# Optimization experiments

Measured on AMD Instinct MI355X. Metric: run time of the kernel, lower is better.

Reference implementation:

```python
import jax, jax.numpy as jnp
import numpy as np

B, T, C = 1, 2048, 1024
H, D = 16, 64  # n_head, head_size (n_query_groups == n_head -> plain MHA)


def build_rope_cache(seq_len, n_elem, base=10000):
    theta = 1.0 / (base ** (jnp.arange(0, n_elem, 2, dtype=jnp.float32) / n_elem))
    idx_theta = jnp.outer(jnp.arange(seq_len, dtype=jnp.float32), theta)
    idx_theta = jnp.concatenate([idx_theta, idx_theta], axis=-1)  # torch .repeat(1, 2)
    return jnp.cos(idx_theta), jnp.sin(idx_theta)


def apply_rope(x, cos, sin):
    d = x.shape[-1]
    x1, x2 = x[..., : d // 2], x[..., d // 2 :]
    rotated = jnp.concatenate([-x2, x1], axis=-1)
    return x * cos + rotated * sin


def fastmax_attention(q, k, v):
    """Fastmax: first-order Taylor approx of softmax attention, causal, O(n*d^2).
    score(i,j) = 1 + q_i . k_j (temperature=1, zero RPE, no dropout);
    out_i = sum_{j<=i} score*v_j / sum_{j<=i} score, via causal cumulative sums."""
    n = q.shape[2]
    kcum = jnp.cumsum(k, axis=2)                                       # (B,H,T,D)
    kvcum = jnp.cumsum(jnp.einsum('bhnd,bhne->bhnde', k, v), axis=2)   # (B,H,T,D,D)
    den = jnp.arange(1, n + 1, dtype=q.dtype) + jnp.einsum('bhnd,bhnd->bhn', q, kcum)
    num = jnp.cumsum(v, axis=2) + jnp.einsum('bhnd,bhnde->bhne', q, kvcum)
    return num / den[..., None]


def setup_inputs() -> dict:
    key = jax.random.key(0)
    k1, k2, k3 = jax.random.split(key, 3)
    scale = 0.02
    x = jax.random.normal(k1, (B, T, C), dtype=jnp.float32)
    w_attn = jax.random.normal(k2, (3 * H * D, C), dtype=jnp.float32) * scale
    w_proj = jax.random.normal(k3, (C, H * D), dtype=jnp.float32) * scale
    cos, sin = build_rope_cache(T, D)
    return {"x": x, "w_attn": w_attn, "w_proj": w_proj, "cos": cos, "sin": sin}


def reference(x, w_attn, w_proj, cos, sin):
    Bx, Tx, Cx = x.shape
    qkv = x @ w_attn.T                                  # (B,T,3HD)
    qkv = qkv.reshape(Bx, Tx, H, 3, D).transpose(0, 2, 3, 1, 4)  # (B,H,3,T,D)
    q, k, v = qkv[:, :, 0], qkv[:, :, 1], qkv[:, :, 2]
    q = apply_rope(q, cos, sin)
    k = apply_rope(k, cos, sin)
    y = fastmax_attention(q, k, v)                      # (B,H,T,D)
    y = y.transpose(0, 2, 1, 3).reshape(Bx, Tx, H * D)
    return y @ w_proj.T
```

## Files before the change

kernel.cpp:

```cpp
#include <hip/hip_runtime.h>

#define T_LEN 2048
#define C_DIM 1024
#define H_NUM 16
#define D_DIM 64
#define QKV_N (3 * H_NUM * D_DIM)
#define L_CHK 64
#define NC (T_LEN / L_CHK)

typedef _Float16 h8 __attribute__((ext_vector_type(8)));
typedef _Float16 h4 __attribute__((ext_vector_type(4)));
typedef float f32x4 __attribute__((ext_vector_type(4)));

__global__ __launch_bounds__(256) void split3_f16(
    const float* __restrict__ x, _Float16* __restrict__ xh,
    _Float16* __restrict__ xl, const float* __restrict__ wa,
    _Float16* __restrict__ wah, _Float16* __restrict__ wal,
    const float* __restrict__ wp, _Float16* __restrict__ wph) {
  int i = (blockIdx.x * 256 + threadIdx.x) * 8;
  const float* src;
  _Float16 *dh, *dl = nullptr;
  int base;
  if (i < 2097152) {
    src = x; dh = xh; dl = xl; base = i;
  } else if (i < 2097152 + 3145728) {
    src = wa; dh = wah; dl = wal; base = i - 2097152;
  } else {
    src = wp; dh = wph; base = i - 5242880;
  }
  float4 a = *(const float4*)(src + base);
  float4 b = *(const float4*)(src + base + 4);
  float v[8] = {a.x, a.y, a.z, a.w, b.x, b.y, b.z, b.w};
  h8 hv, lv;
#pragma unroll
  for (int j = 0; j < 8; ++j) {
    float s = v[j] * 64.f;
    _Float16 h = (_Float16)s;
    hv[j] = h;
    lv[j] = (_Float16)(s - (float)h);
  }
  *(h8*)(dh + base) = hv;
  if (dl) *(h8*)(dl + base) = lv;
}

__device__ __forceinline__ void split8(float4 a, float4 b, h8& hi, h8& lo) {
  float v[8] = {a.x, a.y, a.z, a.w, b.x, b.y, b.z, b.w};
#pragma unroll
  for (int m = 0; m < 8; ++m) {
    _Float16 hh = (_Float16)v[m];
    hi[m] = hh;
    lo[m] = (_Float16)(v[m] - (float)hh);
  }
}

template <int BN, bool ROPE, bool SPLIT3>
__global__ __launch_bounds__(256) void gemm_nt_f16(
    const _Float16* __restrict__ Ah, const _Float16* __restrict__ Al,
    const _Float16* __restrict__ Bh, const _Float16* __restrict__ Bl,
    float* __restrict__ C, const float* __restrict__ cosb,
    const float* __restrict__ sinb, _Float16* __restrict__ qh_,
    _Float16* __restrict__ ql_, _Float16* __restrict__ kh_,
    _Float16* __restrict__ kl_, _Float16* __restrict__ kTh_,
    _Float16* __restrict__ kTl_, _Float16* __restrict__ vTh_,
    int M, int N, int K, float outscale) {
  constexpr int NJ = BN / 32;
  constexpr int NARR = SPLIT3 ? 2 : 1;
  constexpr int GEMM_BYTES = (64 * 64 * 2 + BN * 64 * 2) * NARR;
  constexpr int ROPE_BYTES = ROPE ? (2 * 64 * 36 * 4 + 2 * 64 * 64 * 4) : 0;
  constexpr int SMEM_BYTES = GEMM_BYTES > ROPE_BYTES ? GEMM_BYTES : ROPE_BYTES;
  __shared__ __align__(16) char smem[SMEM_BYTES];
  _Float16* sAh = (_Float16*)smem;
  _Float16* sAl = sAh + 64 * 64;
  _Float16* sBh = sAh + 64 * 64 * NARR;
  _Float16* sBl = sBh + BN * 64;
  const int tid = threadIdx.x;
  const int wave = tid >> 6;
  const int lane = tid & 63;
  const int bm = blockIdx.y * 64;
  const int bn = blockIdx.x * BN;
  const int wm = wave >> 1;
  const int wn = wave & 1;
  const int srow = lane >> 3;
  const int sblk = ((lane & 7) ^ srow) * 8;
  const int quad = lane >> 4;
  const int lrow = lane & 15;

  f32x4 acc[2][NJ];
#pragma unroll
  for (int i = 0; i < 2; ++i)
#pragma unroll
    for (int j = 0; j < NJ; ++j) acc[i][j] = (f32x4){0.f, 0.f, 0.f, 0.f};

  for (int k0 = 0; k0 < K; k0 += 64) {
#pragma unroll
    for (int it = 0; it < 2; ++it) {
      const int ch = wave + it * 4;
      const int row = ch * 8 + srow;
      const _Float16* ga = Ah + (size_t)(bm + row) * K + k0 + sblk;
      __builtin_amdgcn_global_load_lds(
          (const __attribute__((address_space(1))) void*)ga,
          (__attribute__((address_space(3))) void*)(sAh + ch * 512), 16, 0, 0);
      if constexpr (SPLIT3) {
        const _Float16* gb = Al + (size_t)(bm + row) * K + k0 + sblk;
        __builtin_amdgcn_global_load_lds(
            (const __attribute__((address_space(1))) void*)gb,
            (__attribute__((address_space(3))) void*)(sAl + ch * 512), 16, 0,
            0);
      }
    }
#pragma unroll
    for (int it = 0; it < BN / 32; ++it) {
      const int ch = wave + it * 4;
      const int row = ch * 8 + srow;
      const _Float16* ga = Bh + (size_t)(bn + row) * K + k0 + sblk;
      __builtin_amdgcn_global_load_lds(
          (const __attribute__((address_space(1))) void*)ga,
          (__attribute__((address_space(3))) void*)(sBh + ch * 512), 16, 0, 0);
      if constexpr (SPLIT3) {
        const _Float16* gb = Bl + (size_t)(bn + row) * K + k0 + sblk;
        __builtin_amdgcn_global_load_lds(
            (const __attribute__((address_space(1))) void*)gb,
            (__attribute__((address_space(3))) void*)(sBl + ch * 512), 16, 0,
            0);
      }
    }
    __syncthreads();
#pragma unroll
    for (int kk = 0; kk < 2; ++kk) {
      h8 ah[2], al[2], bh[NJ], bl[NJ];
#pragma unroll
      for (int i = 0; i < 2; ++i) {
        const int row = wm * 32 + i * 16 + lrow;
        const int ra = row * 64 + (((kk * 4 + quad) ^ (row & 7)) * 8);
        ah[i] = *(const h8*)&sAh[ra];
        if constexpr (SPLIT3) al[i] = *(const h8*)&sAl[ra];
      }
#pragma unroll
      for (int j = 0; j < NJ; ++j) {
        const int row = wn * (BN / 2) + j * 16 + lrow;
        const int rb = row * 64 + (((kk * 4 + quad) ^ (row & 7)) * 8);
        bh[j] = *(const h8*)&sBh[rb];
        if constexpr (SPLIT3) bl[j] = *(const h8*)&sBl[rb];
      }
#pragma unroll
      for (int i = 0; i < 2; ++i)
#pragma unroll
        for (int j = 0; j < NJ; ++j) {
          acc[i][j] = __builtin_amdgcn_mfma_f32_16x16x32_f16(
              ah[i], bh[j], acc[i][j], 0, 0, 0);
          if constexpr (SPLIT3) {
            acc[i][j] = __builtin_amdgcn_mfma_f32_16x16x32_f16(
                ah[i], bl[j], acc[i][j], 0, 0, 0);
            acc[i][j] = __builtin_amdgcn_mfma_f32_16x16x32_f16(
                al[i], bh[j], acc[i][j], 0, 0, 0);
          }
        }
    }
    __syncthreads();
  }
  if constexpr (!ROPE) {
#pragma unroll
    for (int i = 0; i < 2; ++i) {
      const int rbase = bm + wm * 32 + i * 16 + quad * 4;
#pragma unroll
      for (int j = 0; j < NJ; ++j) {
        const int col = bn + wn * (BN / 2) + j * 16 + lrow;
#pragma unroll
        for (int r = 0; r < 4; ++r)
          C[(size_t)(rbase + r) * N + col] = acc[i][j][r] * outscale;
      }
    }
  } else {
    float* cs = (float*)smem;
    float* sn = cs + 2304;
    float* bounce = sn + 2304;
    {
      const int el = tid * 8;
      const int t = el >> 5, d0 = el & 31;
      const float* gc = &cosb[(size_t)(bm + t) * D_DIM + d0];
      const float* gs = &sinb[(size_t)(bm + t) * D_DIM + d0];
      *(float4*)&cs[t * 36 + d0] = *(const float4*)gc;
      *(float4*)&cs[t * 36 + d0 + 4] = *(const float4*)(gc + 4);
      *(float4*)&sn[t * 36 + d0] = *(const float4*)gs;
      *(float4*)&sn[t * 36 + d0 + 4] = *(const float4*)(gs + 4);
    }
    __syncthreads();
    const int colbase = bn + wn * 64;
    const int type = (colbase >> 6) % 3;
    const int head = colbase / 192;
    const size_t hb = (size_t)head * T_LEN * D_DIM;
    float fv[2][4][4];
#pragma unroll
    for (int i = 0; i < 2; ++i)
#pragma unroll
      for (int r = 0; r < 4; ++r) {
        const int tloc = wm * 32 + i * 16 + quad * 4 + r;
#pragma unroll
        for (int j = 0; j < 4; ++j) {
          const int d32 = (j & 1) * 16 + lrow;
          float val = acc[i][j][r] * outscale;
          if (type < 2) {
            float rotv =
                ((j < 2) ? -acc[i][j + 2][r] : acc[i][j - 2][r]) * outscale;
            val = val * cs[tloc * 36 + d32] + rotv * sn[tloc * 36 + d32];
          }
          fv[i][r][j] = val;
        }
      }
    if (type < 2) {
      _Float16* dh = (type == 0 ? qh_ : kh_) + hb;
      _Float16* dl = (type == 0 ? ql_ : kl_) + hb;
#pragma unroll
      for (int i = 0; i < 2; ++i)
#pragma unroll
        for (int r = 0; r < 4; ++r) {
          const size_t trow =
              (size_t)(bm + wm * 32 + i * 16 + quad * 4 + r) * D_DIM;
#pragma unroll
          for (int j = 0; j < 4; ++j) {
            const int d = j * 16 + lrow;
            float f = fv[i][r][j];
            _Float16 hh = (_Float16)f;
            dh[trow + d] = hh;
            dl[trow + d] = (_Float16)(f - (float)hh);
          }
        }
    }
    const bool doT = (type >= 1);
    _Float16* th = (type == 1 ? kTh_ : vTh_) + hb;
    _Float16* tl = kTl_ + hb;
    float* myb = bounce + wn * 4096;
    if (doT) {
#pragma unroll
      for (int i = 0; i < 2; ++i)
#pragma unroll
        for (int r = 0; r < 4; ++r) {
          const int tloc = wm * 32 + i * 16 + quad * 4 + r;
#pragma unroll
          for (int j = 0; j < 4; ++j) {
            const int d = j * 16 + lrow;
            myb[tloc * 64 + (d ^ tloc)] = fv[i][r][j];
          }
        }
    }
    __syncthreads();
    if (doT) {
      const int lt = wm * 64 + lane;
      const int e = lt >> 1;
      const int tg0 = (lt & 1) * 32;
#pragma unroll
      for (int s8 = 0; s8 < 4; ++s8) {
        h8 hv, lv;
#pragma unroll
        for (int s = 0; s < 8; ++s) {
          const int t = tg0 + s8 * 8 + s;
          float f = myb[t * 64 + (e ^ t)];
          _Float16 hh = (_Float16)f;
          hv[s] = hh;
          lv[s] = (_Float16)(f - (float)hh);
        }
        *(h8*)&th[(size_t)e * T_LEN + bm + tg0 + s8 * 8] = hv;
        if (type == 1)
          *(h8*)&tl[(size_t)e * T_LEN + bm + tg0 + s8 * 8] = lv;
      }
    }
  }
}

__global__ __launch_bounds__(256) void chunk_kvT(
    const _Float16* __restrict__ kTh, const _Float16* __restrict__ kTl,
    const _Float16* __restrict__ vTh, float* __restrict__ kvchunk,
    float* __restrict__ kschunk, float* __restrict__ vschunk) {
  const int blk = blockIdx.x;
  const int h = blk / NC, c = blk % NC;
  const int tid = threadIdx.x;
  const int wave = tid >> 6, lane = tid & 63;
  const int quad = lane >> 4, lrow = lane & 15;
  const size_t hb = (size_t)h * D_DIM * T_LEN;
  const int tb = c * L_CHK;
  h8 avh[2];
  {
    const _Float16* pa = vTh + hb + (size_t)(wave * 16 + lrow) * T_LEN + tb +
                         quad * 8;
    avh[0] = *(const h8*)pa;
    avh[1] = *(const h8*)(pa + 32);
  }
  f32x4 accv[4];
#pragma unroll
  for (int dt = 0; dt < 4; ++dt) accv[dt] = (f32x4){0.f, 0.f, 0.f, 0.f};
#pragma unroll
  for (int dt = 0; dt < 4; ++dt) {
    const _Float16* pb = kTh + hb + (size_t)(dt * 16 + lrow) * T_LEN + tb +
                         quad * 8;
#pragma unroll
    for (int ks = 0; ks < 2; ++ks) {
      h8 bh = *(const h8*)(pb + ks * 32);
      accv[dt] = __builtin_amdgcn_mfma_f32_16x16x32_f16(avh[ks], bh, accv[dt],
                                                        0, 0, 0);
    }
  }
  float* ob = kvchunk + (size_t)blk * (D_DIM * D_DIM);
#pragma unroll
  for (int dt = 0; dt < 4; ++dt)
#pragma unroll
    for (int r = 0; r < 4; ++r)
      ob[(wave * 16 + quad * 4 + r) * D_DIM + dt * 16 + lrow] = accv[dt][r];
  if (tid < 64) {
    const _Float16* p = kTh + hb + (size_t)tid * T_LEN + tb;
    const _Float16* pl = kTl + hb + (size_t)tid * T_LEN + tb;
    float s = 0.f;
#pragma unroll
    for (int i = 0; i < 8; ++i) {
      h8 a = *(const h8*)(p + i * 8), b = *(const h8*)(pl + i * 8);
#pragma unroll
      for (int m = 0; m < 8; ++m) s += (float)a[m] + (float)b[m];
    }
    kschunk[(size_t)blk * D_DIM + tid] = s;
  } else if (tid < 128) {
    const int e = tid - 64;
    const _Float16* p = vTh + hb + (size_t)e * T_LEN + tb;
    float s = 0.f;
#pragma unroll
    for (int i = 0; i < 8; ++i) {
      h8 a = *(const h8*)(p + i * 8);
#pragma unroll
      for (int m = 0; m < 8; ++m) s += (float)a[m];
    }
    vschunk[(size_t)blk * D_DIM + e] = s;
  }
}

__global__ __launch_bounds__(256) void scan_fused(
    const float* __restrict__ kvchunk, _Float16* __restrict__ kvph,
    const float* __restrict__ kschunk, const float* __restrict__ vschunk,
    float* __restrict__ kspref, float* __restrict__ vspref) {
  int b = blockIdx.x;
  int tid = threadIdx.x;
  if (b < 256) {
    int gid = b * 256 + tid;
    int h = gid >> 12;
    int de = gid & 4095;
    float vals[NC];
#pragma unroll
    for (int c = 0; c < NC; ++c)
      vals[c] = kvchunk[((size_t)(h * NC + c) << 12) + de];
    float run = 0.f;
#pragma unroll
    for (int c = 0; c < NC; ++c) {
      kvph[((size_t)(h * NC + c) << 12) + de] = (_Float16)run;
      run += vals[c];
    }
  } else {
    int gid = (b - 256) * 256 + tid;
    int h = gid >> 6, d = gid & 63;
    float kv_[NC], vv_[NC];
#pragma unroll
    for (int c = 0; c < NC; ++c) {
      size_t idx = (size_t)(h * NC + c) * 64 + d;
      kv_[c] = kschunk[idx];
      vv_[c] = vschunk[idx];
    }
    float rk = 0.f, rv = 0.f;
#pragma unroll
    for (int c = 0; c < NC; ++c) {
      size_t idx = (size_t)(h * NC + c) * 64 + d;
      kspref[idx] = rk;
      vspref[idx] = rv;
      rk += kv_[c];
      rv += vv_[c];
    }
  }
}

__global__ __launch_bounds__(256) void attn_mfma(
    const _Float16* __restrict__ qh, const _Float16* __restrict__ ql,
    const _Float16* __restrict__ kh, const _Float16* __restrict__ kl,
    const _Float16* __restrict__ vTh, const _Float16* __restrict__ kvph,
    const float* __restrict__ kspref, const float* __restrict__ vspref,
    _Float16* __restrict__ yh) {
  __shared__ __align__(16) _Float16 sS[2][4][16 * 64];
  const int blk = blockIdx.x;
  const int h = blk / NC, c = blk % NC;
  const int tid = threadIdx.x;
  const int wave = tid >> 6, lane = tid & 63;
  const int quad = lane >> 4, lrow = lane & 15;
  const size_t hb = (size_t)h * T_LEN * D_DIM;
  const size_t hbT = (size_t)h * D_DIM * T_LEN;
  const int t0 = c * L_CHK;
  const f32x4 z4 = {0.f, 0.f, 0.f, 0.f};
  h8 aqh[2], aql[2];
  {
    const _Float16* pq =
        qh + hb + (size_t)(t0 + wave * 16 + lrow) * D_DIM + quad * 8;
    const _Float16* pql =
        ql + hb + (size_t)(t0 + wave * 16 + lrow) * D_DIM + quad * 8;
    aqh[0] = *(const h8*)pq;
    aqh[1] = *(const h8*)(pq + 32);
    aql[0] = *(const h8*)pql;
    aql[1] = *(const h8*)(pql + 32);
  }
  f32x4 sacc[4];
#pragma unroll
  for (int jt = 0; jt < 4; ++jt) sacc[jt] = z4;
#pragma unroll
  for (int jt = 0; jt < 4; ++jt) {
    const _Float16* pk =
        kh + hb + (size_t)(t0 + jt * 16 + lrow) * D_DIM + quad * 8;
    const _Float16* pkl =
        kl + hb + (size_t)(t0 + jt * 16 + lrow) * D_DIM + quad * 8;
#pragma unroll
    for (int ks = 0; ks < 2; ++ks) {
      h8 bh = *(const h8*)(pk + ks * 32);
      h8 bl = *(const h8*)(pkl + ks * 32);
      sacc[jt] = __builtin_amdgcn_mfma_f32_16x16x32_f16(aqh[ks], bh, sacc[jt],
                                                        0, 0, 0);
      sacc[jt] = __builtin_amdgcn_mfma_f32_16x16x32_f16(aqh[ks], bl, sacc[jt],
                                                        0, 0, 0);
      sacc[jt] = __builtin_amdgcn_mfma_f32_16x16x32_f16(aql[ks], bh, sacc[jt],
                                                        0, 0, 0);
    }
  }
  _Float16* shp = &sS[0][wave][0];
  _Float16* slp = &sS[1][wave][0];
#pragma unroll
  for (int jt = 0; jt < 4; ++jt)
#pragma unroll
    for (int r = 0; r < 4; ++r) {
      const int row = quad * 4 + r;
      const int j = jt * 16 + lrow;
      const int rglob = wave * 16 + row;
      float s = (j <= rglob) ? (sacc[jt][r] + 1.f) : 0.f;
      _Float16 hh = (_Float16)s;
      const int adr = row * 64 + ((((j >> 3) ^ (row & 7)) << 3) | (j & 7));
      shp[adr] = hh;
      slp[adr] = (_Float16)(s - (float)hh);
    }
  h8 ash[2], asl[2];
#pragma unroll
  for (int ks = 0; ks < 2; ++ks) {
    const int adr = lrow * 64 + (((ks * 4 + quad) ^ (lrow & 7)) << 3);
    ash[ks] = *(const h8*)&shp[adr];
    asl[ks] = *(const h8*)&slp[adr];
  }
  h8 ones;
#pragma unroll
  for (int m = 0; m < 8; ++m) ones[m] = (_Float16)1.0f;
  f32x4 rs = z4;
#pragma unroll
  for (int ks = 0; ks < 2; ++ks) {
    rs = __builtin_amdgcn_mfma_f32_16x16x32_f16(ash[ks], ones, rs, 0, 0, 0);
    rs = __builtin_amdgcn_mfma_f32_16x16x32_f16(asl[ks], ones, rs, 0, 0, 0);
  }
  f32x4 oacc[4];
#pragma unroll
  for (int et = 0; et < 4; ++et) oacc[et] = z4;
#pragma unroll
  for (int et = 0; et < 4; ++et) {
    const _Float16* pv =
        vTh + hbT + (size_t)(et * 16 + lrow) * T_LEN + t0 + quad * 8;
#pragma unroll
    for (int ks = 0; ks < 2; ++ks) {
      h8 bh = *(const h8*)(pv + ks * 32);
      oacc[et] = __builtin_amdgcn_mfma_f32_16x16x32_f16(ash[ks], bh, oacc[et],
                                                        0, 0, 0);
      oacc[et] = __builtin_amdgcn_mfma_f32_16x16x32_f16(asl[ks], bh, oacc[et],
                                                        0, 0, 0);
    }
  }
  const _Float16* kvp = kvph + ((size_t)blk << 12);
#pragma unroll
  for (int et = 0; et < 4; ++et) {
#pragma unroll
    for (int ks = 0; ks < 2; ++ks) {
      h8 bh = *(const h8*)&kvp[(et * 16 + lrow) * D_DIM + ks * 32 + quad * 8];
      oacc[et] = __builtin_amdgcn_mfma_f32_16x16x32_f16(aqh[ks], bh, oacc[et],
                                                        0, 0, 0);
    }
  }
  const float* ksp = kspref + (size_t)blk * D_DIM;
  f32x4 kacc = z4;
#pragma unroll
  for (int ks = 0; ks < 2; ++ks) {
    const float* pb = ksp + ks * 32 + quad * 8;
    float4 b0 = *(const float4*)pb;
    float4 b1 = *(const float4*)(pb + 4);
    h8 bh, bl;
    split8(b0, b1, bh, bl);
    kacc = __builtin_amdgcn_mfma_f32_16x16x32_f16(aqh[ks], bh, kacc, 0, 0, 0);
    kacc = __builtin_amdgcn_mfma_f32_16x16x32_f16(aqh[ks], bl, kacc, 0, 0, 0);
    kacc = __builtin_amdgcn_mfma_f32_16x16x32_f16(aql[ks], bh, kacc, 0, 0, 0);
  }
  const float* vsp = vspref + (size_t)blk * D_DIM;
#pragma unroll
  for (int r = 0; r < 4; ++r) {
    const int row = wave * 16 + quad * 4 + r;
    const float den = (float)(c * L_CHK) + rs[r] + kacc[r];
    const float inv = 1.f / den;
    const size_t ybase = (size_t)(t0 + row) * (H_NUM * D_DIM) + h * D_DIM;
#pragma unroll
    for (int et = 0; et < 4; ++et) {
      const int e = et * 16 + lrow;
      const float num = oacc[et][r] + vsp[e];
      yh[ybase + e] = (_Float16)(num * inv);
    }
  }
}

extern "C" void kernel_launch(void* const* d_in, const int* in_sizes, int n_in,
                              void* d_out, int out_size, void* d_ws,
                              size_t ws_size, hipStream_t stream) {
  const float* x = (const float*)d_in[0];
  const float* w_attn = (const float*)d_in[1];
  const float* w_proj = (const float*)d_in[2];
  const float* cosb = (const float*)d_in[3];
  const float* sinb = (const float*)d_in[4];
  float* out = (float*)d_out;

  char* ws = (char*)d_ws;
  const size_t MB = 1048576;
  float* kvchunk = (float*)ws;
  _Float16* kvph = (_Float16*)(ws + 8 * MB);
  _Float16* qh = (_Float16*)(ws + 16 * MB);
  _Float16* ql = (_Float16*)(ws + 20 * MB);
  _Float16* kh = (_Float16*)(ws + 24 * MB);
  _Float16* kl = (_Float16*)(ws + 28 * MB);
  _Float16* kTh = (_Float16*)(ws + 32 * MB);
  _Float16* kTl = (_Float16*)(ws + 36 * MB);
  _Float16* vTh = (_Float16*)(ws + 40 * MB);
  _Float16* xh = (_Float16*)(ws + 48 * MB);
  _Float16* xl = (_Float16*)(ws + 52 * MB);
  _Float16* yh = (_Float16*)(ws + 48 * MB);
  _Float16* wah = (_Float16*)(ws + 56 * MB);
  _Float16* wal = (_Float16*)(ws + 62 * MB);
  float* kschunk = (float*)(ws + 56 * MB);
  float* vschunk = (float*)(ws + 56 * MB + 131072);
  float* kspref = (float*)(ws + 56 * MB + 262144);
  float* vspref = (float*)(ws + 56 * MB + 393216);
  _Float16* wph = (_Float16*)(ws + 68 * MB);

  split3_f16<<<3072, 256, 0, stream>>>(x, xh, xl, w_attn, wah, wal, w_proj,
                                       wph);

  {
    dim3 grid(QKV_N / 128, T_LEN / 64);
    gemm_nt_f16<128, true, true><<<grid, 256, 0, stream>>>(
        xh, xl, wah, wal, nullptr, cosb, sinb, qh, ql, kh, kl, kTh, kTl, vTh,
        T_LEN, QKV_N, C_DIM, 1.f / 4096.f);
  }
  chunk_kvT<<<H_NUM * NC, 256, 0, stream>>>(kTh, kTl, vTh, kvchunk, kschunk,
                                            vschunk);
  scan_fused<<<260, 256, 0, stream>>>(kvchunk, kvph, kschunk, vschunk,
                                      kspref, vspref);
  attn_mfma<<<H_NUM * NC, 256, 0, stream>>>(qh, ql, kh, kl, vTh, kvph,
                                            kspref, vspref, yh);
  {
    dim3 grid(C_DIM / 64, T_LEN / 64);
    gemm_nt_f16<64, false, false><<<grid, 256, 0, stream>>>(
        yh, nullptr, wph, nullptr, out, nullptr, nullptr, nullptr, nullptr,
        nullptr, nullptr, nullptr, nullptr, nullptr, T_LEN, C_DIM, C_DIM,
        1.f / 64.f);
  }
}
```

Before: 161.2 us.

## Group QKV GEMM tiles by type and skip split-precision work for V

Each QKV GEMM block's column tiles are remapped so a block covers one projection type (Q, K or V) for two heads. V blocks then skip the low-part loads and the two extra correction MFMAs, using only the high-part product. V blocks also skip the cos/sin load, and the transpose barrier now sits inside the branch. The output-projection GEMM moves to 128-wide N tiles. V loses the compensated precision, and the output GEMM now launches fewer, larger blocks.

```diff
diff --git a/kernel.cpp b/kernel.cpp
--- a/kernel.cpp
+++ b/kernel.cpp
@@ -77,13 +77,24 @@
   const int wave = tid >> 6;
   const int lane = tid & 63;
   const int bm = blockIdx.y * 64;
-  const int bn = blockIdx.x * BN;
   const int wm = wave >> 1;
   const int wn = wave & 1;
   const int srow = lane >> 3;
   const int sblk = ((lane & 7) ^ srow) * 8;
   const int quad = lane >> 4;
   const int lrow = lane & 15;
+
+  int btype = -1, pi = 0, cb0, cb1;
+  if constexpr (ROPE) {
+    btype = blockIdx.x >> 3;
+    pi = blockIdx.x & 7;
+    cb0 = (2 * pi) * 3 + btype;
+    cb1 = (2 * pi + 1) * 3 + btype;
+  } else {
+    cb0 = blockIdx.x * (BN / 64);
+    cb1 = cb0 + 1;
+  }
+  const bool isV = ROPE && (btype == 2);
 
   f32x4 acc[2][NJ];
 #pragma unroll
@@ -101,60 +112,88 @@
           (const __attribute__((address_space(1))) void*)ga,
           (__attribute__((address_space(3))) void*)(sAh + ch * 512), 16, 0, 0);
       if constexpr (SPLIT3) {
-        const _Float16* gb = Al + (size_t)(bm + row) * K + k0 + sblk;
-        __builtin_amdgcn_global_load_lds(
-            (const __attribute__((address_space(1))) void*)gb,
-            (__attribute__((address_space(3))) void*)(sAl + ch * 512), 16, 0,
-            0);
+        if (!isV) {
+          const _Float16* gb = Al + (size_t)(bm + row) * K + k0 + sblk;
+          __builtin_amdgcn_global_load_lds(
+              (const __attribute__((address_space(1))) void*)gb,
+              (__attribute__((address_space(3))) void*)(sAl + ch * 512), 16, 0,
+              0);
+        }
       }
     }
 #pragma unroll
     for (int it = 0; it < BN / 32; ++it) {
       const int ch = wave + it * 4;
-      const int row = ch * 8 + srow;
-      const _Float16* ga = Bh + (size_t)(bn + row) * K + k0 + sblk;
+      const int lr = ch * 8 + srow;
+      const int grow = ((lr < 64) ? cb0 : cb1) * 64 + (lr & 63);
+      const _Float16* ga = Bh + (size_t)grow * K + k0 + sblk;
       __builtin_amdgcn_global_load_lds(
           (const __attribute__((address_space(1))) void*)ga,
           (__attribute__((address_space(3))) void*)(sBh + ch * 512), 16, 0, 0);
       if constexpr (SPLIT3) {
-        const _Float16* gb = Bl + (size_t)(bn + row) * K + k0 + sblk;
-        __builtin_amdgcn_global_load_lds(
-            (const __attribute__((address_space(1))) void*)gb,
-            (__attribute__((address_space(3))) void*)(sBl + ch * 512), 16, 0,
-            0);
+        if (!isV) {
+          const _Float16* gb = Bl + (size_t)grow * K + k0 + sblk;
+          __builtin_amdgcn_global_load_lds(
+              (const __attribute__((address_space(1))) void*)gb,
+              (__attribute__((address_space(3))) void*)(sBl + ch * 512), 16, 0,
+              0);
+        }
       }
     }
     __syncthreads();
-#pragma unroll
-    for (int kk = 0; kk < 2; ++kk) {
-      h8 ah[2], al[2], bh[NJ], bl[NJ];
-#pragma unroll
-      for (int i = 0; i < 2; ++i) {
-        const int row = wm * 32 + i * 16 + lrow;
-        const int ra = row * 64 + (((kk * 4 + quad) ^ (row & 7)) * 8);
-        ah[i] = *(const h8*)&sAh[ra];
-        if constexpr (SPLIT3) al[i] = *(const h8*)&sAl[ra];
-      }
-#pragma unroll
-      for (int j = 0; j < NJ; ++j) {
-        const int row = wn * (BN / 2) + j * 16 + lrow;
-        const int rb = row * 64 + (((kk * 4 + quad) ^ (row & 7)) * 8);
-        bh[j] = *(const h8*)&sBh[rb];
-        if constexpr (SPLIT3) bl[j] = *(const h8*)&sBl[rb];
-      }
-#pragma unroll
-      for (int i = 0; i < 2; ++i)
+    if (SPLIT3 && !isV) {
+#pragma unroll
+      for (int kk = 0; kk < 2; ++kk) {
+        h8 ah[2], al[2], bh[NJ], bl[NJ];
+#pragma unroll
+        for (int i = 0; i < 2; ++i) {
+          const int row = wm * 32 + i * 16 + lrow;
+          const int ra = row * 64 + (((kk * 4 + quad) ^ (row & 7)) * 8);
+          ah[i] = *(const h8*)&sAh[ra];
+          al[i] = *(const h8*)&sAl[ra];
+        }
 #pragma unroll
         for (int j = 0; j < NJ; ++j) {
-          acc[i][j] = __builtin_amdgcn_mfma_f32_16x16x32_f16(
-              ah[i], bh[j], acc[i][j], 0, 0, 0);
-          if constexpr (SPLIT3) {
+          const int row = wn * (BN / 2) + j * 16 + lrow;
+          const int rb = row * 64 + (((kk * 4 + quad) ^ (row & 7)) * 8);
+          bh[j] = *(const h8*)&sBh[rb];
+          bl[j] = *(const h8*)&sBl[rb];
+        }
+#pragma unroll
+        for (int i = 0; i < 2; ++i)
+#pragma unroll
+          for (int j = 0; j < NJ; ++j) {
+            acc[i][j] = __builtin_amdgcn_mfma_f32_16x16x32_f16(
+                ah[i], bh[j], acc[i][j], 0, 0, 0);
             acc[i][j] = __builtin_amdgcn_mfma_f32_16x16x32_f16(
                 ah[i], bl[j], acc[i][j], 0, 0, 0);
             acc[i][j] = __builtin_amdgcn_mfma_f32_16x16x32_f16(
                 al[i], bh[j], acc[i][j], 0, 0, 0);
           }
-        }
+      }
+    } else {
+#pragma unroll
+      for (int kk = 0; kk < 2; ++kk) {
+        h8 ah[2], bh[NJ];
+#pragma unroll
+        for (int i = 0; i < 2; ++i) {
+          const int row = wm * 32 + i * 16 + lrow;
+          const int ra = row * 64 + (((kk * 4 + quad) ^ (row & 7)) * 8);
+          ah[i] = *(const h8*)&sAh[ra];
+        }
+#pragma unroll
+        for (int j = 0; j < NJ; ++j) {
+          const int row = wn * (BN / 2) + j * 16 + lrow;
+          const int rb = row * 64 + (((kk * 4 + quad) ^ (row & 7)) * 8);
+          bh[j] = *(const h8*)&sBh[rb];
+        }
+#pragma unroll
+        for (int i = 0; i < 2; ++i)
+#pragma unroll
+          for (int j = 0; j < NJ; ++j)
+            acc[i][j] = __builtin_amdgcn_mfma_f32_16x16x32_f16(
+                ah[i], bh[j], acc[i][j], 0, 0, 0);
+      }
     }
     __syncthreads();
   }
@@ -164,7 +203,7 @@
       const int rbase = bm + wm * 32 + i * 16 + quad * 4;
 #pragma unroll
       for (int j = 0; j < NJ; ++j) {
-        const int col = bn + wn * (BN / 2) + j * 16 + lrow;
+        const int col = blockIdx.x * BN + wn * (BN / 2) + j * 16 + lrow;
 #pragma unroll
         for (int r = 0; r < 4; ++r)
           C[(size_t)(rbase + r) * N + col] = acc[i][j][r] * outscale;
@@ -174,7 +213,7 @@
     float* cs = (float*)smem;
     float* sn = cs + 2304;
     float* bounce = sn + 2304;
-    {
+    if (btype < 2) {
       const int el = tid * 8;
       const int t = el >> 5, d0 = el & 31;
       const float* gc = &cosb[(size_t)(bm + t) * D_DIM + d0];
@@ -185,9 +224,7 @@
       *(float4*)&sn[t * 36 + d0 + 4] = *(const float4*)(gs + 4);
     }
     __syncthreads();
-    const int colbase = bn + wn * 64;
-    const int type = (colbase >> 6) % 3;
-    const int head = colbase / 192;
+    const int head = 2 * pi + wn;
     const size_t hb = (size_t)head * T_LEN * D_DIM;
     float fv[2][4][4];
 #pragma unroll
@@ -199,7 +236,7 @@
         for (int j = 0; j < 4; ++j) {
           const int d32 = (j & 1) * 16 + lrow;
           float val = acc[i][j][r] * outscale;
-          if (type < 2) {
+          if (btype < 2) {
             float rotv =
                 ((j < 2) ? -acc[i][j + 2][r] : acc[i][j - 2][r]) * outscale;
             val = val * cs[tloc * 36 + d32] + rotv * sn[tloc * 36 + d32];
@@ -207,9 +244,9 @@
           fv[i][r][j] = val;
         }
       }
-    if (type < 2) {
-      _Float16* dh = (type == 0 ? qh_ : kh_) + hb;
-      _Float16* dl = (type == 0 ? ql_ : kl_) + hb;
+    if (btype < 2) {
+      _Float16* dh = (btype == 0 ? qh_ : kh_) + hb;
+      _Float16* dl = (btype == 0 ? ql_ : kl_) + hb;
 #pragma unroll
       for (int i = 0; i < 2; ++i)
 #pragma unroll
@@ -226,11 +263,10 @@
           }
         }
     }
-    const bool doT = (type >= 1);
-    _Float16* th = (type == 1 ? kTh_ : vTh_) + hb;
-    _Float16* tl = kTl_ + hb;
-    float* myb = bounce + wn * 4096;
-    if (doT) {
+    if (btype >= 1) {
+      _Float16* th = (btype == 1 ? kTh_ : vTh_) + hb;
+      _Float16* tl = kTl_ + hb;
+      float* myb = bounce + wn * 4096;
 #pragma unroll
       for (int i = 0; i < 2; ++i)
 #pragma unroll
@@ -242,9 +278,7 @@
             myb[tloc * 64 + (d ^ tloc)] = fv[i][r][j];
           }
         }
-    }
-    __syncthreads();
-    if (doT) {
+      __syncthreads();
       const int lt = wm * 64 + lane;
       const int e = lt >> 1;
       const int tg0 = (lt & 1) * 32;
@@ -260,7 +294,7 @@
           lv[s] = (_Float16)(f - (float)hh);
         }
         *(h8*)&th[(size_t)e * T_LEN + bm + tg0 + s8 * 8] = hv;
-        if (type == 1)
+        if (btype == 1)
           *(h8*)&tl[(size_t)e * T_LEN + bm + tg0 + s8 * 8] = lv;
       }
     }
@@ -554,8 +588,8 @@
   attn_mfma<<<H_NUM * NC, 256, 0, stream>>>(qh, ql, kh, kl, vTh, kvph,
                                             kspref, vspref, yh);
   {
-    dim3 grid(C_DIM / 64, T_LEN / 64);
-    gemm_nt_f16<64, false, false><<<grid, 256, 0, stream>>>(
+    dim3 grid(C_DIM / 128, T_LEN / 64);
+    gemm_nt_f16<128, false, false><<<grid, 256, 0, stream>>>(
         yh, nullptr, wph, nullptr, out, nullptr, nullptr, nullptr, nullptr,
         nullptr, nullptr, nullptr, nullptr, nullptr, T_LEN, C_DIM, C_DIM,
         1.f / 64.f);
```

Result: no change. 159.1 us (-1.3%).
